# Kernel tuning notes

Measured on AMD Instinct MI355X. Metric: run time of the kernel, lower is better.

The kernel has to match this reference:

```python
import jax, jax.numpy as jnp
import numpy as np

B = 512        # graphs per batch
N_NODES = 64   # nodes per graph
IN_CH = 256
EMBED = 64
TOPK = 20
NEG_SLOPE = 0.2


def setup_inputs() -> dict:
    key = jax.random.key(0)
    ks = jax.random.split(key, 6)
    N = B * N_NODES
    x = jax.random.normal(ks[0], (N, IN_CH), dtype=jnp.float32)
    # fully-connected graph WITH self loops, per graph, sorted source-major
    src = jnp.repeat(jnp.arange(N_NODES, dtype=jnp.int32), N_NODES)  # [n*n]
    dst = jnp.tile(jnp.arange(N_NODES, dtype=jnp.int32), N_NODES)    # [n*n]
    offs = (jnp.arange(B, dtype=jnp.int32) * N_NODES)[:, None]       # [B,1]
    l = (src[None, :] + offs).reshape(-1)
    r = (dst[None, :] + offs).reshape(-1)
    edge_index = jnp.stack([l, r]).astype(jnp.int32)                 # [2, B*n*n]
    batch = jnp.repeat(jnp.arange(B, dtype=jnp.int32), N_NODES)      # [N]
    glorot = lambda k, sh: jax.random.uniform(k, sh, jnp.float32,
                                              -1.0, 1.0) * np.sqrt(6.0 / (sh[0] + sh[-1]))
    Wl = glorot(ks[1], (EMBED, IN_CH))
    bl = jnp.zeros((EMBED,), jnp.float32)
    Wr = glorot(ks[2], (EMBED, IN_CH))
    br = jnp.zeros((EMBED,), jnp.float32)
    att = glorot(ks[3], (1, EMBED))
    return {"x": x, "edge_index": edge_index, "batch": batch,
            "Wl": Wl, "bl": bl, "Wr": Wr, "br": br, "att": att}


def reference(x, edge_index, batch, Wl, bl, Wr, br, att):
    N = x.shape[0]
    x_l = x @ Wl.T + bl                      # [N, D]
    x_r = x @ Wr.T + br                      # [N, D]
    l, r = edge_index[0], edge_index[1]
    # edge gather + GAT-style score
    e = jax.nn.leaky_relu(x_l[l] + x_r[r], negative_slope=NEG_SLOPE)  # [E, D]
    alpha = (e * att[0]).sum(axis=-1)                                  # [E]
    # segment softmax grouped by source node l (each group is non-empty)
    m = jax.ops.segment_max(alpha, l, num_segments=N)
    a = jnp.exp(alpha - m[l])
    s = jax.ops.segment_sum(a, l, num_segments=N)
    a = a / s[l]
    # kNN sparsify: zero the diagonal then per-row topk
    a3 = a.reshape(B, N_NODES, N_NODES)
    a3 = a3 * (1.0 - jnp.eye(N_NODES, dtype=a3.dtype))
    attention, indices = jax.lax.top_k(a3, TOPK)     # [B, n, k] sorted desc
    attention = attention.reshape(-1)                 # [B*n*k]
    offs = (jnp.arange(B, dtype=jnp.int32) * N_NODES)[:, None]
    index_i = (jnp.repeat(jnp.arange(N_NODES, dtype=jnp.int32), TOPK)[None, :]
               + offs).reshape(-1)
    index_j = (indices.astype(jnp.int32)
               + (jnp.arange(B, dtype=jnp.int32) * N_NODES)[:, None, None]).reshape(-1)
    new_edge_index = jnp.stack([index_i, index_j])    # [2, B*n*k]
    return new_edge_index, attention
```

## Files before the change

### kernel.cpp

```cpp
#include <hip/hip_runtime.h>
#include <stdint.h>

#define NGRAPH 512
#define NN 64
#define INCH 256
#define TOPK 20
#define EPR 655360
#define WS_NEED ((size_t)65536 + (size_t)16777216)

typedef __attribute__((ext_vector_type(8))) short bf16x8;
typedef __attribute__((ext_vector_type(4))) float f32x4;

#define XLR 0
#define XRR 4352
#define SMEM_DW 8704

static __device__ __forceinline__ uint32_t f2bfbits(float f) {
  uint32_t u = __float_as_uint(f);
  return (u + 0x7FFFu + ((u >> 16) & 1u)) >> 16;
}
static __device__ __forceinline__ uint32_t pk2(float a, float b) {
  return f2bfbits(a) | (f2bfbits(b) << 16);
}
static __device__ __forceinline__ float keyalpha(uint32_t k) {
  uint32_t ub = (k & 0x80000000u) ? (k ^ 0x80000000u) : ~k;
  return __uint_as_float(ub & 0xFFFFFFC0u);
}
static __device__ __forceinline__ float redsum64(float v) {
  int p;
  p = __builtin_amdgcn_update_dpp(0, __float_as_int(v), 0xB1, 0xF, 0xF, true);
  v += __int_as_float(p);
  p = __builtin_amdgcn_update_dpp(0, __float_as_int(v), 0x4E, 0xF, 0xF, true);
  v += __int_as_float(p);
  v += __shfl_xor(v, 4);
  v += __shfl_xor(v, 8);
  v += __shfl_xor(v, 16);
  v += __shfl_xor(v, 32);
  return v;
}

__global__ __launch_bounds__(256) void wpack2(const float* __restrict__ Wl,
                                              const float* __restrict__ Wr,
                                              uint4* __restrict__ wsW) {
  const int t = blockIdx.x * 256 + threadIdx.x;
  const int lo = t & 15, quad = (t >> 4) & 3, ct = (t >> 6) & 3;
  const int ks = (t >> 8) & 7, half = (t >> 11) & 1;
  const int n = ct * 16 + lo, k0 = ks * 32 + quad * 8;
  const float* src = half ? Wr : Wl;
  const float4* s4 = (const float4*)(src + (size_t)n * INCH + k0);
  float4 a0 = s4[0], a1 = s4[1];
  wsW[t] = (uint4){ pk2(a0.x, a0.y), pk2(a0.z, a0.w), pk2(a1.x, a1.y), pk2(a1.z, a1.w) };
}

__global__ __launch_bounds__(256) void xpack(const float* __restrict__ x,
                                             uint4* __restrict__ xp) {
  const int t = blockIdx.x * 256 + threadIdx.x;
  const int lo = t & 15, quad = (t >> 4) & 3, rt = (t >> 6) & 3;
  const int ks = (t >> 8) & 7, b = t >> 11;
  const int row = b * 64 + rt * 16 + lo, k0 = ks * 32 + quad * 8;
  const float4* s4 = (const float4*)(x + (size_t)row * INCH + k0);
  float4 a0 = s4[0], a1 = s4[1];
  xp[t] = (uint4){ pk2(a0.x, a0.y), pk2(a0.z, a0.w), pk2(a1.x, a1.y), pk2(a1.z, a1.w) };
}

template <bool XP>
__global__ __launch_bounds__(512, 4) void gat_fused(
    const float* __restrict__ x,
    const uint4* __restrict__ wsV,
    const float* __restrict__ blv,
    const float* __restrict__ brv,
    const float* __restrict__ att,
    float* __restrict__ out)
{
  __shared__ __align__(16) uint32_t smemU[SMEM_DW];
  float* smemF = (float*)smemU;

  const int b    = blockIdx.x;
  const int t    = threadIdx.x;
  const int w    = t >> 6;
  const int lane = t & 63;
  const int quad = lane >> 4;
  const int lo   = lane & 15;
  const int nodeBase = b * NN;

  const float attv = att[lane];

  const int half = w >> 2;
  const int rt   = w & 3;
  const int r0   = rt * 16;
  const uint4* xpV = wsV + 4096;

  f32x4 acc[4];
  #pragma unroll
  for (int ct = 0; ct < 4; ++ct) acc[ct] = (f32x4){0.f, 0.f, 0.f, 0.f};

  #pragma unroll
  for (int ks = 0; ks < 8; ++ks) {
    bf16x8 afrag;
    if constexpr (XP) {
      uint4 au = xpV[(size_t)b * 2048 + ks * 256 + rt * 64 + quad * 16 + lo];
      afrag = __builtin_bit_cast(bf16x8, au);
    } else {
      const int k0 = ks * 32 + quad * 8;
      const float* ap = x + (size_t)(nodeBase + r0 + lo) * INCH + k0;
      float4 a0 = *(const float4*)ap;
      float4 a1 = *(const float4*)(ap + 4);
      uint4 au = { pk2(a0.x, a0.y), pk2(a0.z, a0.w), pk2(a1.x, a1.y), pk2(a1.z, a1.w) };
      afrag = __builtin_bit_cast(bf16x8, au);
    }
    #pragma unroll
    for (int ct = 0; ct < 4; ++ct) {
      uint4 bu = wsV[half * 2048 + ks * 256 + ct * 64 + quad * 16 + lo];
      bf16x8 bfrag = __builtin_bit_cast(bf16x8, bu);
      acc[ct] = __builtin_amdgcn_mfma_f32_16x16x32_bf16(afrag, bfrag, acc[ct], 0, 0, 0);
    }
  }

  {
    const float* bias = half ? brv : blv;
    const int dstBase = half ? XRR : XLR;
    #pragma unroll
    for (int ct = 0; ct < 4; ++ct) {
      const int d = ct * 16 + lo;
      const float bb = bias[d];
      #pragma unroll
      for (int rg = 0; rg < 4; ++rg)
        smemF[dstBase + (r0 + quad * 4 + rg) * 68 + d] = acc[ct][rg] + bb;
    }
  }
  __syncthreads();

  const int rB = w * 8;

  float xlv[8];
  #pragma unroll
  for (int q = 0; q < 8; ++q)
    xlv[q] = smemF[XLR + (rB + q) * 68 + lane];

  float sl[8];
  #pragma unroll
  for (int q = 0; q < 8; ++q)
    sl[q] = redsum64(attv * xlv[q]);

  float pacc[8];
  #pragma unroll
  for (int q = 0; q < 8; ++q) pacc[q] = 0.f;
  float srp = 0.f;
  const int xrb = XRR + lane * 68;
  #pragma unroll
  for (int c = 0; c < 4; ++c) {
    f32x4 xrc[4];
    #pragma unroll
    for (int g = 0; g < 4; ++g)
      xrc[g] = *(const f32x4*)&smemF[xrb + c * 16 + g * 4];
    #pragma unroll
    for (int dl = 0; dl < 16; ++dl) {
      const int d = c * 16 + dl;
      const float xv = xrc[dl >> 2][dl & 3];
      const float av = __int_as_float(
          __builtin_amdgcn_readlane(__float_as_int(attv), d));
      srp = fmaf(av, xv, srp);
      #pragma unroll
      for (int q = 0; q < 8; ++q) {
        const float xls = __int_as_float(
            __builtin_amdgcn_readlane(__float_as_int(xlv[q]), d));
        pacc[q] = fmaf(av, fabsf(xls + xv), pacc[q]);
      }
    }
  }

  float aq[8];
  #pragma unroll
  for (int q = 0; q < 8; ++q)
    aq[q] = 0.6f * (sl[q] + srp) + 0.4f * pacc[q];

  uint32_t key[8];
  #pragma unroll
  for (int q = 0; q < 8; ++q) {
    const uint32_t u = __float_as_uint(aq[q]);
    uint32_t kk = u ^ ((uint32_t)((int32_t)u >> 31) | 0x80000000u);
    kk = (kk & 0xFFFFFFC0u) | (uint32_t)(63 - lane);
    key[q] = (lane == rB + q) ? 0u : kk;
  }

  #pragma unroll
  for (int k = 2; k <= 64; k <<= 1) {
    #pragma unroll
    for (int j = k >> 1; j >= 1; j >>= 1) {
      const bool keep_max = (((lane & k) == 0) == ((lane & j) == 0));
      #pragma unroll
      for (int q = 0; q < 8; ++q) {
        uint32_t p;
        if (j == 1)
          p = (uint32_t)__builtin_amdgcn_update_dpp(0, (int)key[q], 0xB1, 0xF, 0xF, true);
        else if (j == 2)
          p = (uint32_t)__builtin_amdgcn_update_dpp(0, (int)key[q], 0x4E, 0xF, 0xF, true);
        else
          p = (uint32_t)__shfl_xor((int)key[q], j);
        const uint32_t mx = (key[q] > p) ? key[q] : p;
        const uint32_t mn = (key[q] > p) ? p : key[q];
        key[q] = keep_max ? mx : mn;
      }
    }
  }

  float mq[8], Sq[8];
  #pragma unroll
  for (int q = 0; q < 8; ++q) {
    const uint32_t tk = (uint32_t)__builtin_amdgcn_readlane((int)key[q], 0);
    const float topa  = keyalpha(tk);
    const float adiag = __int_as_float(
        __builtin_amdgcn_readlane(__float_as_int(aq[q]), rB + q));
    mq[q] = fmaxf(topa, adiag);
    Sq[q] = redsum64(__expf(aq[q] - mq[q]));
  }

  if (lane < TOPK) {
    #pragma unroll
    for (int q = 0; q < 8; ++q) {
      const int g = nodeBase + rB + q;
      const uint32_t kq = key[q];
      const float alpha = keyalpha(kq);
      const int jj = 63 - (int)(kq & 63u);
      const float va = __expf(alpha - mq[q]) * (1.0f / Sq[q]);
      out[(size_t)g * 20 + lane] = (float)g;
      out[(size_t)EPR + (size_t)g * 20 + lane] = (float)(nodeBase + jj);
      out[2 * (size_t)EPR + (size_t)g * 20 + lane] = va;
    }
  }
}

extern "C" void kernel_launch(void* const* d_in, const int* in_sizes, int n_in,
                              void* d_out, int out_size, void* d_ws, size_t ws_size,
                              hipStream_t stream) {
  const float* x   = (const float*)d_in[0];
  const float* Wl  = (const float*)d_in[3];
  const float* bl  = (const float*)d_in[4];
  const float* Wr  = (const float*)d_in[5];
  const float* br  = (const float*)d_in[6];
  const float* att = (const float*)d_in[7];
  uint4* wsW = (uint4*)d_ws;

  wpack2<<<dim3(16), dim3(256), 0, stream>>>(Wl, Wr, wsW);
  if (ws_size >= WS_NEED) {
    xpack<<<dim3(4096), dim3(256), 0, stream>>>(x, wsW + 4096);
    gat_fused<true><<<dim3(NGRAPH), dim3(512), 0, stream>>>(
        x, wsW, bl, br, att, (float*)d_out);
  } else {
    gat_fused<false><<<dim3(NGRAPH), dim3(512), 0, stream>>>(
        x, wsW, bl, br, att, (float*)d_out);
  }
}
```

Before: 124.6 us.

## Stage x through swizzled LDS in fused kernel, drop xpack, use permlane butterflies

Removes the separate xpack pre-kernel. Each block now loads its 64x256 fp32 slab of x coalesced, converts it to bf16, and stores it into an XOR-swizzled LDS tile that feeds the MFMA A-fragments. The change also moves the x_l/x_r tiles to a stride of 65, drops the per-row sl reduction by folding the 0.6*sl term out of the scores, reads att directly in the inner loop, and uses DPP row_shr/permlane swap butterflies in the bitonic sort and reductions. The cost is about 64KB of LDS per block, which lowers occupancy. Dropping sl relies on softmax and top-k being invariant to a per-row constant shift.

```diff
diff --git a/kernel.cpp b/kernel.cpp
--- a/kernel.cpp
+++ b/kernel.cpp
@@ -6,14 +6,14 @@
 #define INCH 256
 #define TOPK 20
 #define EPR 655360
-#define WS_NEED ((size_t)65536 + (size_t)16777216)
 
 typedef __attribute__((ext_vector_type(8))) short bf16x8;
 typedef __attribute__((ext_vector_type(4))) float f32x4;
 
-#define XLR 0
-#define XRR 4352
-#define SMEM_DW 8704
+#define XBF 0
+#define XLR 8192
+#define XRR 12352
+#define SMEM_DW 16512
 
 static __device__ __forceinline__ uint32_t f2bfbits(float f) {
   uint32_t u = __float_as_uint(f);
@@ -26,16 +26,38 @@
   uint32_t ub = (k & 0x80000000u) ? (k ^ 0x80000000u) : ~k;
   return __uint_as_float(ub & 0xFFFFFFC0u);
 }
-static __device__ __forceinline__ float redsum64(float v) {
-  int p;
-  p = __builtin_amdgcn_update_dpp(0, __float_as_int(v), 0xB1, 0xF, 0xF, true);
-  v += __int_as_float(p);
-  p = __builtin_amdgcn_update_dpp(0, __float_as_int(v), 0x4E, 0xF, 0xF, true);
-  v += __int_as_float(p);
-  v += __shfl_xor(v, 4);
-  v += __shfl_xor(v, 8);
-  v += __shfl_xor(v, 16);
-  v += __shfl_xor(v, 32);
+
+static __device__ __forceinline__ uint32_t bflyu(uint32_t v, const int j, const int lane) {
+  if (j == 1)
+    return (uint32_t)__builtin_amdgcn_update_dpp(0, (int)v, 0xB1, 0xF, 0xF, true);
+  if (j == 2)
+    return (uint32_t)__builtin_amdgcn_update_dpp(0, (int)v, 0x4E, 0xF, 0xF, true);
+  if (j == 8)
+    return (uint32_t)__builtin_amdgcn_update_dpp(0, (int)v, 0x128, 0xF, 0xF, true);
+#if __has_builtin(__builtin_amdgcn_permlane16_swap)
+  if (j == 16) {
+    auto r = __builtin_amdgcn_permlane16_swap((unsigned)v, (unsigned)v, false, false);
+    return (uint32_t)(((lane >> 4) & 1) ? r[0] : r[1]);
+  }
+#endif
+#if __has_builtin(__builtin_amdgcn_permlane32_swap)
+  if (j == 32) {
+    auto r = __builtin_amdgcn_permlane32_swap((unsigned)v, (unsigned)v, false, false);
+    return (uint32_t)((lane & 32) ? r[0] : r[1]);
+  }
+#endif
+  return (uint32_t)__shfl_xor((int)v, j);
+}
+static __device__ __forceinline__ float bflyf(float v, const int j, const int lane) {
+  return __uint_as_float(bflyu(__float_as_uint(v), j, lane));
+}
+static __device__ __forceinline__ float redsum64(float v, const int lane) {
+  v += bflyf(v, 1, lane);
+  v += bflyf(v, 2, lane);
+  v += bflyf(v, 4, lane);
+  v += bflyf(v, 8, lane);
+  v += bflyf(v, 16, lane);
+  v += bflyf(v, 32, lane);
   return v;
 }
 
@@ -52,19 +74,7 @@
   wsW[t] = (uint4){ pk2(a0.x, a0.y), pk2(a0.z, a0.w), pk2(a1.x, a1.y), pk2(a1.z, a1.w) };
 }
 
-__global__ __launch_bounds__(256) void xpack(const float* __restrict__ x,
-                                             uint4* __restrict__ xp) {
-  const int t = blockIdx.x * 256 + threadIdx.x;
-  const int lo = t & 15, quad = (t >> 4) & 3, rt = (t >> 6) & 3;
-  const int ks = (t >> 8) & 7, b = t >> 11;
-  const int row = b * 64 + rt * 16 + lo, k0 = ks * 32 + quad * 8;
-  const float4* s4 = (const float4*)(x + (size_t)row * INCH + k0);
-  float4 a0 = s4[0], a1 = s4[1];
-  xp[t] = (uint4){ pk2(a0.x, a0.y), pk2(a0.z, a0.w), pk2(a1.x, a1.y), pk2(a1.z, a1.w) };
-}
-
-template <bool XP>
-__global__ __launch_bounds__(512, 4) void gat_fused(
+__global__ __launch_bounds__(512, 4) void gat3(
     const float* __restrict__ x,
     const uint4* __restrict__ wsV,
     const float* __restrict__ blv,
@@ -83,12 +93,22 @@
   const int lo   = lane & 15;
   const int nodeBase = b * NN;
 
-  const float attv = att[lane];
+  {
+    const float* xg = x + (size_t)nodeBase * INCH;
+    #pragma unroll
+    for (int i = 0; i < 8; ++i) {
+      const int fd = i * 2048 + t * 4;
+      float4 v = *(const float4*)(xg + fd);
+      const int row = fd >> 8;
+      const int c2  = (fd & 255) >> 1;
+      const int dw  = row * 128 + (c2 ^ ((row & 7) << 2));
+      *(uint2*)&smemU[XBF + dw] = (uint2){ pk2(v.x, v.y), pk2(v.z, v.w) };
+    }
+  }
+  __syncthreads();
 
   const int half = w >> 2;
-  const int rt   = w & 3;
-  const int r0   = rt * 16;
-  const uint4* xpV = wsV + 4096;
+  const int r0   = (w & 3) * 16;
 
   f32x4 acc[4];
   #pragma unroll
@@ -96,18 +116,9 @@
 
   #pragma unroll
   for (int ks = 0; ks < 8; ++ks) {
-    bf16x8 afrag;
-    if constexpr (XP) {
-      uint4 au = xpV[(size_t)b * 2048 + ks * 256 + rt * 64 + quad * 16 + lo];
-      afrag = __builtin_bit_cast(bf16x8, au);
-    } else {
-      const int k0 = ks * 32 + quad * 8;
-      const float* ap = x + (size_t)(nodeBase + r0 + lo) * INCH + k0;
-      float4 a0 = *(const float4*)ap;
-      float4 a1 = *(const float4*)(ap + 4);
-      uint4 au = { pk2(a0.x, a0.y), pk2(a0.z, a0.w), pk2(a1.x, a1.y), pk2(a1.z, a1.w) };
-      afrag = __builtin_bit_cast(bf16x8, au);
-    }
+    const int adw = XBF + (r0 + lo) * 128 + ((ks * 16 + quad * 4) ^ ((lo & 7) << 2));
+    uint4 au = *(const uint4*)&smemU[adw];
+    bf16x8 afrag = __builtin_bit_cast(bf16x8, au);
     #pragma unroll
     for (int ct = 0; ct < 4; ++ct) {
       uint4 bu = wsV[half * 2048 + ks * 256 + ct * 64 + quad * 16 + lo];
@@ -125,7 +136,7 @@
       const float bb = bias[d];
       #pragma unroll
       for (int rg = 0; rg < 4; ++rg)
-        smemF[dstBase + (r0 + quad * 4 + rg) * 68 + d] = acc[ct][rg] + bb;
+        smemF[dstBase + (r0 + quad * 4 + rg) * 65 + d] = acc[ct][rg] + bb;
     }
   }
   __syncthreads();
@@ -135,18 +146,13 @@
   float xlv[8];
   #pragma unroll
   for (int q = 0; q < 8; ++q)
-    xlv[q] = smemF[XLR + (rB + q) * 68 + lane];
-
-  float sl[8];
-  #pragma unroll
-  for (int q = 0; q < 8; ++q)
-    sl[q] = redsum64(attv * xlv[q]);
+    xlv[q] = smemF[XLR + (rB + q) * 65 + lane];
 
   float pacc[8];
   #pragma unroll
   for (int q = 0; q < 8; ++q) pacc[q] = 0.f;
   float srp = 0.f;
-  const int xrb = XRR + lane * 68;
+  const int xrb = XRR + lane * 65;
   #pragma unroll
   for (int c = 0; c < 4; ++c) {
     f32x4 xrc[4];
@@ -157,14 +163,13 @@
     for (int dl = 0; dl < 16; ++dl) {
       const int d = c * 16 + dl;
       const float xv = xrc[dl >> 2][dl & 3];
-      const float av = __int_as_float(
-          __builtin_amdgcn_readlane(__float_as_int(attv), d));
-      srp = fmaf(av, xv, srp);
+      const float ad = att[d];
+      srp = fmaf(ad, xv, srp);
       #pragma unroll
       for (int q = 0; q < 8; ++q) {
         const float xls = __int_as_float(
             __builtin_amdgcn_readlane(__float_as_int(xlv[q]), d));
-        pacc[q] = fmaf(av, fabsf(xls + xv), pacc[q]);
+        pacc[q] = fmaf(ad, fabsf(xls + xv), pacc[q]);
       }
     }
   }
@@ -172,7 +177,7 @@
   float aq[8];
   #pragma unroll
   for (int q = 0; q < 8; ++q)
-    aq[q] = 0.6f * (sl[q] + srp) + 0.4f * pacc[q];
+    aq[q] = 0.6f * srp + 0.4f * pacc[q];
 
   uint32_t key[8];
   #pragma unroll
@@ -190,13 +195,7 @@
       const bool keep_max = (((lane & k) == 0) == ((lane & j) == 0));
       #pragma unroll
       for (int q = 0; q < 8; ++q) {
-        uint32_t p;
-        if (j == 1)
-          p = (uint32_t)__builtin_amdgcn_update_dpp(0, (int)key[q], 0xB1, 0xF, 0xF, true);
-        else if (j == 2)
-          p = (uint32_t)__builtin_amdgcn_update_dpp(0, (int)key[q], 0x4E, 0xF, 0xF, true);
-        else
-          p = (uint32_t)__shfl_xor((int)key[q], j);
+        const uint32_t p = bflyu(key[q], j, lane);
         const uint32_t mx = (key[q] > p) ? key[q] : p;
         const uint32_t mn = (key[q] > p) ? p : key[q];
         key[q] = keep_max ? mx : mn;
@@ -208,11 +207,10 @@
   #pragma unroll
   for (int q = 0; q < 8; ++q) {
     const uint32_t tk = (uint32_t)__builtin_amdgcn_readlane((int)key[q], 0);
-    const float topa  = keyalpha(tk);
     const float adiag = __int_as_float(
         __builtin_amdgcn_readlane(__float_as_int(aq[q]), rB + q));
-    mq[q] = fmaxf(topa, adiag);
-    Sq[q] = redsum64(__expf(aq[q] - mq[q]));
+    mq[q] = fmaxf(keyalpha(tk), adiag);
+    Sq[q] = redsum64(__expf(aq[q] - mq[q]), lane);
   }
 
   if (lane < TOPK) {
@@ -242,12 +240,5 @@
   uint4* wsW = (uint4*)d_ws;
 
   wpack2<<<dim3(16), dim3(256), 0, stream>>>(Wl, Wr, wsW);
-  if (ws_size >= WS_NEED) {
-    xpack<<<dim3(4096), dim3(256), 0, stream>>>(x, wsW + 4096);
-    gat_fused<true><<<dim3(NGRAPH), dim3(512), 0, stream>>>(
-        x, wsW, bl, br, att, (float*)d_out);
-  } else {
-    gat_fused<false><<<dim3(NGRAPH), dim3(512), 0, stream>>>(
-        x, wsW, bl, br, att, (float*)d_out);
-  }
-}
+  gat3<<<dim3(NGRAPH), dim3(512), 0, stream>>>(x, wsW, bl, br, att, (float*)d_out);
+}
```

Result: faster. 119.4 us (-4.1%).
